# Performance work log

Measured on AMD Instinct MI355X. Metric: run time of the kernel, lower is better.

The kernel has to match this reference:

```python
import jax, jax.numpy as jnp
import numpy as np

N_NODES = 100000
IN_CH, HID_CH, OUT_CH = 128, 128, 64
N_EDGES = 1600000


def gcn_conv(x, W, b, src, dst, num_nodes):
    """PyG GCNConv: x@W -> symmetric-normalized aggregation with self-loops -> +bias."""
    h = x @ W  # [N, out]
    loop = jnp.arange(num_nodes, dtype=src.dtype)
    src_a = jnp.concatenate([src, loop])  # add self-loops
    dst_a = jnp.concatenate([dst, loop])
    # degree of destination nodes over augmented edge set (edge_weight = 1)
    deg = jax.ops.segment_sum(jnp.ones_like(dst_a, dtype=h.dtype), dst_a,
                              num_segments=num_nodes)
    dis = jnp.where(deg > 0, jax.lax.rsqrt(jnp.maximum(deg, 1e-30)), 0.0)
    norm = dis[src_a] * dis[dst_a]  # [E+N]
    msg = h[src_a] * norm[:, None]  # gather + normalize
    out = jax.ops.segment_sum(msg, dst_a, num_segments=num_nodes)  # scatter-add
    return out + b


def setup_inputs() -> dict:
    key = jax.random.key(0)
    ks = jax.random.split(key, 9)
    x = jax.random.normal(ks[0], (N_NODES, IN_CH), dtype=jnp.float32)
    edge_index = jax.random.randint(ks[1], (2, N_EDGES), 0, N_NODES, dtype=jnp.int64)
    def glorot(k, fan_in, fan_out):
        s = np.sqrt(6.0 / (fan_in + fan_out)).astype(np.float32)
        return jax.random.uniform(k, (fan_in, fan_out), jnp.float32, -s, s)
    return {
        "x": x,
        "edge_index": edge_index,
        "W1": glorot(ks[2], IN_CH, HID_CH),
        "b1": jnp.zeros((HID_CH,), jnp.float32),
        "W2": glorot(ks[3], HID_CH, HID_CH),
        "b2": jnp.zeros((HID_CH,), jnp.float32),
        "Wo": glorot(ks[4], HID_CH, OUT_CH),
        "bo": jnp.zeros((OUT_CH,), jnp.float32),
    }


def reference(x, edge_index, W1, b1, W2, b2, Wo, bo):
    src, dst = edge_index[0], edge_index[1]
    n = x.shape[0]
    x1 = jax.nn.relu(gcn_conv(x, W1, b1, src, dst, n))
    x2 = jax.nn.relu(gcn_conv(x1, W2, b2, src, dst, n))
    return (x1 + x2) @ Wo + bo
```

## Files before the change

### kernel.cpp

```cpp
#include <hip/hip_runtime.h>
#include <hip/hip_fp16.h>

#define N_NODES 100000
#define N_EDGES 1600000
#define CH 128
#define OCH 64
#define NBUCKET 391
#define CAP 8192
#define BIN_CHUNK 4096
#define ZROW N_NODES

typedef _Float16 half8 __attribute__((ext_vector_type(8)));
typedef float f32x4 __attribute__((ext_vector_type(4)));

__device__ __forceinline__ ushort f2h(float f) {
    _Float16 h = (_Float16)f;
    return *(ushort*)&h;
}

__device__ __forceinline__ uint pkadd(uint a, uint b) {
    __half2 r = __hadd2(*(__half2*)&a, *(__half2*)&b);
    return *(uint*)&r;
}

__device__ __forceinline__ uint4 pk4(uint4 a, uint4 b) {
    a.x = pkadd(a.x, b.x); a.y = pkadd(a.y, b.y);
    a.z = pkadd(a.z, b.z); a.w = pkadd(a.w, b.w);
    return a;
}

__device__ __forceinline__ int swz(int row, int k) {
    return row * 128 + ((((k >> 3) ^ (row & 15)) << 3) | (k & 7));
}


__global__ __launch_bounds__(512) void k_bin(const int* __restrict__ src,
                                             const int* __restrict__ dst,
                                             int* __restrict__ bfill,
                                             int* __restrict__ bin) {
    __shared__ int hist[512];
    __shared__ int wbase[512];
    __shared__ int cur[512];
    const int t = threadIdx.x;
    const int e0 = blockIdx.x * BIN_CHUNK;

    hist[t] = 0;
    __syncthreads();

    int ss[8], bb[8], dl[8];
#pragma unroll
    for (int j = 0; j < 8; ++j) {
        int e = e0 + j * 512 + t;
        bb[j] = -1;
        if (e < N_EDGES) {
            int s = src[e], d = dst[e];
            ss[j] = s; dl[j] = d & 255; bb[j] = d >> 8;
            atomicAdd(&hist[bb[j]], 1);
        }
    }
    __syncthreads();

    int v = hist[t];
    for (int off = 1; off < 512; off <<= 1) {
        int tv = (t >= off) ? hist[t - off] : 0;
        __syncthreads();
        hist[t] += tv;
        __syncthreads();
    }
    int excl = hist[t] - v;
    if (t < NBUCKET && v > 0) {
        int gb = atomicAdd(&bfill[t], v);
        wbase[t] = gb - excl;
    }
    cur[t] = excl;
    __syncthreads();

#pragma unroll
    for (int j = 0; j < 8; ++j) {
        if (bb[j] >= 0) {
            int p = atomicAdd(&cur[bb[j]], 1);
            bin[bb[j] * CAP + wbase[bb[j]] + p] = (ss[j] << 8) | dl[j];
        }
    }
}

__global__ __launch_bounds__(512) void k_scan_prep(const int* __restrict__ bfill,
                                                   int* __restrict__ bbase,
                                                   const float* __restrict__ W1,
                                                   const float* __restrict__ W2,
                                                   const float* __restrict__ Wo,
                                                   ushort* __restrict__ W1s,
                                                   ushort* __restrict__ W2s,
                                                   ushort* __restrict__ WoTs,
                                                   ushort* __restrict__ h) {
    if (blockIdx.x == 0) {
        __shared__ int tmp[512];
        int t = threadIdx.x;
        int v = (t < NBUCKET) ? bfill[t] : 0;
        tmp[t] = v;
        __syncthreads();
        for (int off = 1; off < 512; off <<= 1) {
            int tv = (t >= off) ? tmp[t - off] : 0;
            __syncthreads();
            tmp[t] += tv;
            __syncthreads();
        }
        if (t < NBUCKET) bbase[t] = tmp[t] - v;
    } else if (blockIdx.x == 81) {
        if (threadIdx.x < CH) h[(size_t)ZROW * CH + threadIdx.x] = 0;
    } else {
        int i = (blockIdx.x - 1) * 512 + threadIdx.x;
        if (i < 16384) {
            int k = i >> 7, n = i & 127;
            W1s[swz(n, k)] = f2h(W1[i]);
        } else if (i < 32768) {
            int j = i - 16384, k = j >> 7, n = j & 127;
            W2s[swz(n, k)] = f2h(W2[j]);
        } else if (i < 40960) {
            int j = i - 32768, k = j >> 6, n = j & 63;
            WoTs[swz(n, k)] = f2h(Wo[j]);
        }
    }
}

__global__ __launch_bounds__(256) void k_build(const int* __restrict__ bfill,
                                               const int* __restrict__ bbase,
                                               const int* __restrict__ bin,
                                               int* __restrict__ esrc,
                                               int2* __restrict__ scnt,
                                               float* __restrict__ dis) {
    __shared__ int cnt_l[256];
    __shared__ int cur_l[256];
    __shared__ int sortbuf[CAP];
    const int t = threadIdx.x;
    const int b = blockIdx.x;
    const int n = bfill[b];
    const int base = bbase[b];
    const int* brec = bin + b * CAP;

    cnt_l[t] = 0;
    __syncthreads();
    for (int i = t; i < n; i += 256)
        atomicAdd(&cnt_l[brec[i] & 255], 1);
    __syncthreads();

    int v = cnt_l[t];
    for (int off = 1; off < 256; off <<= 1) {
        int tv = (t >= off) ? cnt_l[t - off] : 0;
        __syncthreads();
        cnt_l[t] += tv;
        __syncthreads();
    }
    int excl = cnt_l[t] - v;
    int node = b * 256 + t;
    if (node < N_NODES) {
        scnt[node] = make_int2(base + excl, v);
        dis[node] = rsqrtf((float)(v + 1));
    }
    cur_l[t] = excl;
    __syncthreads();

    for (int i = t; i < n; i += 256) {
        int rec = brec[i];
        int p = atomicAdd(&cur_l[rec & 255], 1);
        sortbuf[p] = rec >> 8;
    }
    __syncthreads();
    for (int i = t; i < n; i += 256)
        esrc[base + i] = sortbuf[i];
}


template <typename IT>
__global__ __launch_bounds__(256) void k_gemm_mfma(const IT* __restrict__ A,
                                                   const ushort* __restrict__ Ws,
                                                   const float* __restrict__ dis,
                                                   ushort* __restrict__ out) {
    __shared__ ushort sB[128 * 128];
    __shared__ ushort sA[64 * 136];
    const int tid = threadIdx.x;
    const int row0 = blockIdx.x * 64;

    for (int i = tid; i < 2048; i += 256)
        ((float4*)sB)[i] = ((const float4*)Ws)[i];

    for (int i = tid; i < 2048; i += 256) {
        int m = i >> 5, u = i & 31, k4 = u << 2;
        int r = row0 + m;
        ushort4 pk = make_ushort4(0, 0, 0, 0);
        if (r < N_NODES) {
            if constexpr (sizeof(IT) == 4) {
                float4 a = ((const float4*)A)[r * 32 + u];
                pk = make_ushort4(f2h(a.x), f2h(a.y), f2h(a.z), f2h(a.w));
            } else {
                pk = ((const ushort4*)A)[r * 32 + u];
            }
        }
        *(ushort4*)&sA[swz(m, k4)] = pk;
    }
    __syncthreads();

    const int lane = tid & 63, wv = tid >> 6;
    const int mrow = lane & 15, quad = lane >> 4;
    f32x4 acc[8] = {};
#pragma unroll
    for (int kc = 0; kc < 4; ++kc) {
        int g = kc * 4 + quad;
        half8 a = *(const half8*)&sA[(wv * 16 + mrow) * 128 + ((g ^ mrow) << 3)];
#pragma unroll
        for (int nt = 0; nt < 8; ++nt) {
            half8 b = *(const half8*)&sB[(nt * 16 + mrow) * 128 + ((g ^ mrow) << 3)];
            acc[nt] = __builtin_amdgcn_mfma_f32_16x16x32_f16(a, b, acc[nt], 0, 0, 0);
        }
    }

    const int rbase4 = wv * 16 + quad * 4;
    float ds[4];
#pragma unroll
    for (int rg = 0; rg < 4; ++rg)
        ds[rg] = (row0 + rbase4 + rg < N_NODES) ? dis[row0 + rbase4 + rg] : 0.f;

    __syncthreads();
#pragma unroll
    for (int nt = 0; nt < 8; ++nt) {
#pragma unroll
        for (int rg = 0; rg < 4; ++rg)
            sA[(rbase4 + rg) * 136 + nt * 16 + mrow] = f2h(acc[nt][rg] * ds[rg]);
    }
    __syncthreads();

#pragma unroll
    for (int k = 0; k < 4; ++k) {
        int idx = tid + k * 256;
        int m = idx >> 4, c16 = idx & 15;
        int r = row0 + m;
        if (r < N_NODES) {
            uint4 vv = *(const uint4*)&sA[m * 136 + c16 * 8];
            ((uint4*)out)[(size_t)r * 16 + c16] = vv;
        }
    }
}


struct Ictx { int n; int grp; int s0, s1, s2, s3, s4, s5; };
struct Gt { uint4 t0, t1, t2, t3, t4, t5, slf; };

__device__ __forceinline__ Ictx idx_stage(const int* __restrict__ esrc, int off, int n, int q) {
    Ictx c; c.n = n;
    const int* ep = esrc + off;
    int r0 = ep[q], r1 = ep[q + 4], r2 = ep[q + 8];
    int r3 = ep[q + 12], r4 = ep[q + 16], r5 = ep[q + 20];
    bool grp = (q + 12 < n);
    bool ok = (n <= q + 24);
    c.grp = grp;
    c.s0 = (grp || q < n)      ? r0 : ZROW;
    c.s1 = (grp || q + 4 < n)  ? r1 : ZROW;
    c.s2 = (grp || q + 8 < n)  ? r2 : ZROW;
    c.s3 = grp                 ? r3 : ZROW;
    c.s4 = (grp && ok && q + 16 < n) ? r4 : ZROW;
    c.s5 = (grp && ok && q + 20 < n) ? r5 : ZROW;
    return c;
}

__device__ __forceinline__ Gt gather_stage(const Ictx& c, int v, int l,
                                           const uint4* __restrict__ h16) {
    Gt g;
    g.t0 = h16[(size_t)c.s0 * 16 + l];
    g.t1 = h16[(size_t)c.s1 * 16 + l];
    g.t2 = h16[(size_t)c.s2 * 16 + l];
    g.t3 = h16[(size_t)c.s3 * 16 + l];
    g.t4 = h16[(size_t)c.s4 * 16 + l];
    g.t5 = h16[(size_t)c.s5 * 16 + l];
    g.slf = h16[(size_t)v * 16 + l];
    return g;
}

__device__ __forceinline__ void acc_finish(const Gt& g, const Ictx& c, int v, int q, int l,
                                           const int* __restrict__ esrc, int off,
                                           const uint4* __restrict__ h16,
                                           float dsv, float4 b0, float4 b1,
                                           ushort* __restrict__ out) {
    uint4 aA = make_uint4(0, 0, 0, 0), aB = make_uint4(0, 0, 0, 0);
    aA = pk4(aA, g.t0);
    if (c.grp) aB = pk4(aB, g.t1); else aA = pk4(aA, g.t1);
    aA = pk4(aA, g.t2);
    if (c.grp) aB = pk4(aB, g.t3); else aA = pk4(aA, g.t3);
    aA = pk4(aA, g.t4);
    aA = pk4(aA, g.t5);
    if (c.n > q + 24) {
        const int* ep = esrc + off;
        int i = q + 16;
        for (; i + 12 < c.n; i += 16) {
            uint4 u0 = h16[(size_t)ep[i] * 16 + l];
            uint4 u1 = h16[(size_t)ep[i + 4] * 16 + l];
            uint4 u2 = h16[(size_t)ep[i + 8] * 16 + l];
            uint4 u3 = h16[(size_t)ep[i + 12] * 16 + l];
            aA = pk4(aA, u0); aB = pk4(aB, u1); aA = pk4(aA, u2); aB = pk4(aB, u3);
        }
        for (; i < c.n; i += 4) aA = pk4(aA, h16[(size_t)ep[i] * 16 + l]);
    }
    aA = pk4(aA, aB);
    aA.x = pkadd(aA.x, (uint)__shfl_xor((int)aA.x, 16));
    aA.y = pkadd(aA.y, (uint)__shfl_xor((int)aA.y, 16));
    aA.z = pkadd(aA.z, (uint)__shfl_xor((int)aA.z, 16));
    aA.w = pkadd(aA.w, (uint)__shfl_xor((int)aA.w, 16));
    aA.x = pkadd(aA.x, (uint)__shfl_xor((int)aA.x, 32));
    aA.y = pkadd(aA.y, (uint)__shfl_xor((int)aA.y, 32));
    aA.z = pkadd(aA.z, (uint)__shfl_xor((int)aA.z, 32));
    aA.w = pkadd(aA.w, (uint)__shfl_xor((int)aA.w, 32));

    if (q == 0) {
        aA = pk4(aA, g.slf);
        float2 a0 = __half22float2(*(__half2*)&aA.x);
        float2 a1 = __half22float2(*(__half2*)&aA.y);
        float2 a2 = __half22float2(*(__half2*)&aA.z);
        float2 a3 = __half22float2(*(__half2*)&aA.w);
        a0.x = fmaxf(a0.x * dsv + b0.x, 0.f); a0.y = fmaxf(a0.y * dsv + b0.y, 0.f);
        a1.x = fmaxf(a1.x * dsv + b0.z, 0.f); a1.y = fmaxf(a1.y * dsv + b0.w, 0.f);
        a2.x = fmaxf(a2.x * dsv + b1.x, 0.f); a2.y = fmaxf(a2.y * dsv + b1.y, 0.f);
        a3.x = fmaxf(a3.x * dsv + b1.z, 0.f); a3.y = fmaxf(a3.y * dsv + b1.w, 0.f);
        __half2 o0 = __float22half2_rn(a0);
        __half2 o1 = __float22half2_rn(a1);
        __half2 o2 = __float22half2_rn(a2);
        __half2 o3 = __float22half2_rn(a3);
        ((uint4*)out)[v * 16 + l] =
            make_uint4(*(uint*)&o0, *(uint*)&o1, *(uint*)&o2, *(uint*)&o3);
    }
}

__global__ __launch_bounds__(256) void k_agg(const int2* __restrict__ scnt,
                                             const int* __restrict__ esrc,
                                             const ushort* __restrict__ h,
                                             const float* __restrict__ dis,
                                             const float* __restrict__ bias,
                                             ushort* __restrict__ out) {
    const int w = threadIdx.x >> 6;
    const int vb = blockIdx.x * 16 + w * 4;
    const int lane = threadIdx.x & 63, q = lane >> 4, l = lane & 15;
    const uint4* h16 = (const uint4*)h;

    int2 m0 = scnt[vb], m1 = scnt[vb + 1], m2 = scnt[vb + 2], m3 = scnt[vb + 3];
    float d0 = dis[vb], d1 = dis[vb + 1], d2 = dis[vb + 2], d3 = dis[vb + 3];
    float4 b0 = ((const float4*)bias)[2 * l];
    float4 b1 = ((const float4*)bias)[2 * l + 1];

    Ictx c0 = idx_stage(esrc, m0.x, m0.y, q);
    Gt g0 = gather_stage(c0, vb, l, h16);
    Ictx c1 = idx_stage(esrc, m1.x, m1.y, q);
    Gt g1 = gather_stage(c1, vb + 1, l, h16);
    Ictx c2 = idx_stage(esrc, m2.x, m2.y, q);
    acc_finish(g0, c0, vb, q, l, esrc, m0.x, h16, d0, b0, b1, out);
    Gt g2 = gather_stage(c2, vb + 2, l, h16);
    Ictx c3 = idx_stage(esrc, m3.x, m3.y, q);
    acc_finish(g1, c1, vb + 1, q, l, esrc, m1.x, h16, d1, b0, b1, out);
    Gt g3 = gather_stage(c3, vb + 3, l, h16);
    acc_finish(g2, c2, vb + 2, q, l, esrc, m2.x, h16, d2, b0, b1, out);
    acc_finish(g3, c3, vb + 3, q, l, esrc, m3.x, h16, d3, b0, b1, out);
}


__global__ __launch_bounds__(256) void k_final_mfma(const ushort* __restrict__ x1,
                                                    const ushort* __restrict__ x2,
                                                    const ushort* __restrict__ Ws,
                                                    const float* __restrict__ bo,
                                                    float* __restrict__ out) {
    __shared__ ushort sB[64 * 128];
    __shared__ ushort sA[64 * 128];
    const int tid = threadIdx.x;
    const int row0 = blockIdx.x * 64;

    for (int i = tid; i < 1024; i += 256)
        ((float4*)sB)[i] = ((const float4*)Ws)[i];

    for (int i = tid; i < 2048; i += 256) {
        int m = i >> 5, u = i & 31, k4 = u << 2;
        int r = row0 + m;
        uint2 pk = make_uint2(0, 0);
        if (r < N_NODES) {
            uint2 ua = ((const uint2*)x1)[r * 32 + u];
            uint2 ub = ((const uint2*)x2)[r * 32 + u];
            __half2 s0 = __hadd2(*(__half2*)&ua.x, *(__half2*)&ub.x);
            __half2 s1 = __hadd2(*(__half2*)&ua.y, *(__half2*)&ub.y);
            pk = make_uint2(*(uint*)&s0, *(uint*)&s1);
        }
        *(uint2*)&sA[swz(m, k4)] = pk;
    }
    __syncthreads();

    const int lane = tid & 63, wv = tid >> 6;
    const int mrow = lane & 15, quad = lane >> 4;
    f32x4 acc[4] = {};
#pragma unroll
    for (int kc = 0; kc < 4; ++kc) {
        int g = kc * 4 + quad;
        half8 a = *(const half8*)&sA[(wv * 16 + mrow) * 128 + ((g ^ mrow) << 3)];
#pragma unroll
        for (int nt = 0; nt < 4; ++nt) {
            half8 b = *(const half8*)&sB[(nt * 16 + mrow) * 128 + ((g ^ mrow) << 3)];
            acc[nt] = __builtin_amdgcn_mfma_f32_16x16x32_f16(a, b, acc[nt], 0, 0, 0);
        }
    }

    const int rbase = row0 + wv * 16 + quad * 4;
#pragma unroll
    for (int nt = 0; nt < 4; ++nt) {
        float bb = bo[nt * 16 + mrow];
#pragma unroll
        for (int rg = 0; rg < 4; ++rg) {
            int r = rbase + rg;
            if (r < N_NODES) out[(size_t)r * 64 + nt * 16 + mrow] = acc[nt][rg] + bb;
        }
    }
}


extern "C" void kernel_launch(void* const* d_in, const int* in_sizes, int n_in,
                              void* d_out, int out_size, void* d_ws, size_t ws_size,
                              hipStream_t stream) {
    const float* x  = (const float*)d_in[0];
    const int*   ei = (const int*)d_in[1];
    const int*   src = ei;
    const int*   dst = ei + N_EDGES;
    const float* W1 = (const float*)d_in[2];
    const float* b1 = (const float*)d_in[3];
    const float* W2 = (const float*)d_in[4];
    const float* b2 = (const float*)d_in[5];
    const float* Wo = (const float*)d_in[6];
    const float* bo = (const float*)d_in[7];
    float* out = (float*)d_out;

    char* ws = (char*)d_ws;
    int*    bfill  = (int*)ws;            ws += 2048;
    int*    bbase  = (int*)ws;            ws += 2048;
    int2*   scnt   = (int2*)ws;           ws += 800000;
    float*  dis    = (float*)ws;          ws += 400000;
    int*    bin    = (int*)ws;            ws += (size_t)NBUCKET * CAP * 4;
    int*    esrc   = (int*)ws;            ws += (size_t)N_EDGES * 4;
    ushort* W1s    = (ushort*)ws;         ws += 32768;
    ushort* W2s    = (ushort*)ws;         ws += 32768;
    ushort* WoTs   = (ushort*)ws;         ws += 16384;
    ushort* h      = (ushort*)ws;         ws += (size_t)(N_NODES + 1) * CH * 2;
    ushort* x1     = (ushort*)ws;         ws += (size_t)N_NODES * CH * 2;
    ushort* x2     = (ushort*)ws;

    const int B = 256;
    const int gG = (N_NODES + 63) / 64;
    const int gA = N_NODES / 16;

    hipMemsetAsync(bfill, 0, 2048, stream);
    k_bin<<<(N_EDGES + BIN_CHUNK - 1) / BIN_CHUNK, 512, 0, stream>>>(src, dst, bfill, bin);
    k_scan_prep<<<82, 512, 0, stream>>>(bfill, bbase, W1, W2, Wo, W1s, W2s, WoTs, h);
    k_build<<<NBUCKET, 256, 0, stream>>>(bfill, bbase, bin, esrc, scnt, dis);

    k_gemm_mfma<float><<<gG, B, 0, stream>>>(x, W1s, dis, h);
    k_agg<<<gA, B, 0, stream>>>(scnt, esrc, h, dis, b1, x1);

    k_gemm_mfma<ushort><<<gG, B, 0, stream>>>(x1, W2s, dis, h);
    k_agg<<<gA, B, 0, stream>>>(scnt, esrc, h, dis, b2, x2);

    k_final_mfma<<<gG, B, 0, stream>>>(x1, x2, WoTs, bo, out);
}
```

Measured before the change: 311.4 us.

## Double GEMM row tile to 128 with 512 threads; stage final output through LDS

The dense GEMM kernels now process 128 rows per block with 512 threads, which halves the number of blocks and the per-block reloads of the weight matrix into shared memory. The final projection kernel also stages its fp32 results through shared memory, so global stores become full 16-byte row writes instead of scattered 4-byte writes. The cost is more shared memory per block (about 67KB for the GEMM), which may lower occupancy, plus an extra LDS round trip and barrier in the final kernel.

```diff
diff --git a/kernel.cpp b/kernel.cpp
--- a/kernel.cpp
+++ b/kernel.cpp
@@ -172,19 +172,19 @@
 
 
 template <typename IT>
-__global__ __launch_bounds__(256) void k_gemm_mfma(const IT* __restrict__ A,
+__global__ __launch_bounds__(512) void k_gemm_mfma(const IT* __restrict__ A,
                                                    const ushort* __restrict__ Ws,
                                                    const float* __restrict__ dis,
                                                    ushort* __restrict__ out) {
     __shared__ ushort sB[128 * 128];
-    __shared__ ushort sA[64 * 136];
+    __shared__ ushort sA[128 * 136];
     const int tid = threadIdx.x;
-    const int row0 = blockIdx.x * 64;
-
-    for (int i = tid; i < 2048; i += 256)
+    const int row0 = blockIdx.x * 128;
+
+    for (int i = tid; i < 2048; i += 512)
         ((float4*)sB)[i] = ((const float4*)Ws)[i];
 
-    for (int i = tid; i < 2048; i += 256) {
+    for (int i = tid; i < 4096; i += 512) {
         int m = i >> 5, u = i & 31, k4 = u << 2;
         int r = row0 + m;
         ushort4 pk = make_ushort4(0, 0, 0, 0);
@@ -231,7 +231,7 @@
 
 #pragma unroll
     for (int k = 0; k < 4; ++k) {
-        int idx = tid + k * 256;
+        int idx = tid + k * 512;
         int m = idx >> 4, c16 = idx & 15;
         int r = row0 + m;
         if (r < N_NODES) {
@@ -359,20 +359,21 @@
 }
 
 
-__global__ __launch_bounds__(256) void k_final_mfma(const ushort* __restrict__ x1,
+__global__ __launch_bounds__(512) void k_final_mfma(const ushort* __restrict__ x1,
                                                     const ushort* __restrict__ x2,
                                                     const ushort* __restrict__ Ws,
                                                     const float* __restrict__ bo,
                                                     float* __restrict__ out) {
     __shared__ ushort sB[64 * 128];
-    __shared__ ushort sA[64 * 128];
+    __shared__ float sF[128 * 68];
+    ushort* sA = (ushort*)sF;
     const int tid = threadIdx.x;
-    const int row0 = blockIdx.x * 64;
-
-    for (int i = tid; i < 1024; i += 256)
+    const int row0 = blockIdx.x * 128;
+
+    for (int i = tid; i < 1024; i += 512)
         ((float4*)sB)[i] = ((const float4*)Ws)[i];
 
-    for (int i = tid; i < 2048; i += 256) {
+    for (int i = tid; i < 4096; i += 512) {
         int m = i >> 5, u = i & 31, k4 = u << 2;
         int r = row0 + m;
         uint2 pk = make_uint2(0, 0);
@@ -401,14 +402,25 @@
         }
     }
 
-    const int rbase = row0 + wv * 16 + quad * 4;
+    const int rbase4 = wv * 16 + quad * 4;
+    __syncthreads();
 #pragma unroll
     for (int nt = 0; nt < 4; ++nt) {
         float bb = bo[nt * 16 + mrow];
 #pragma unroll
-        for (int rg = 0; rg < 4; ++rg) {
-            int r = rbase + rg;
-            if (r < N_NODES) out[(size_t)r * 64 + nt * 16 + mrow] = acc[nt][rg] + bb;
+        for (int rg = 0; rg < 4; ++rg)
+            sF[(rbase4 + rg) * 68 + nt * 16 + mrow] = acc[nt][rg] + bb;
+    }
+    __syncthreads();
+
+#pragma unroll
+    for (int k = 0; k < 4; ++k) {
+        int idx = tid + k * 512;
+        int m = idx >> 4, c16 = idx & 15;
+        int r = row0 + m;
+        if (r < N_NODES) {
+            uint4 vv = *(const uint4*)&sF[m * 68 + c16 * 4];
+            ((uint4*)out)[(size_t)r * 16 + c16] = vv;
         }
     }
 }
@@ -443,8 +455,7 @@
     ushort* x1     = (ushort*)ws;         ws += (size_t)N_NODES * CH * 2;
     ushort* x2     = (ushort*)ws;
 
-    const int B = 256;
-    const int gG = (N_NODES + 63) / 64;
+    const int gG = (N_NODES + 127) / 128;
     const int gA = N_NODES / 16;
 
     hipMemsetAsync(bfill, 0, 2048, stream);
@@ -452,11 +463,11 @@
     k_scan_prep<<<82, 512, 0, stream>>>(bfill, bbase, W1, W2, Wo, W1s, W2s, WoTs, h);
     k_build<<<NBUCKET, 256, 0, stream>>>(bfill, bbase, bin, esrc, scnt, dis);
 
-    k_gemm_mfma<float><<<gG, B, 0, stream>>>(x, W1s, dis, h);
-    k_agg<<<gA, B, 0, stream>>>(scnt, esrc, h, dis, b1, x1);
-
-    k_gemm_mfma<ushort><<<gG, B, 0, stream>>>(x1, W2s, dis, h);
-    k_agg<<<gA, B, 0, stream>>>(scnt, esrc, h, dis, b2, x2);
-
-    k_final_mfma<<<gG, B, 0, stream>>>(x1, x2, WoTs, bo, out);
-}
+    k_gemm_mfma<float><<<gG, 512, 0, stream>>>(x, W1s, dis, h);
+    k_agg<<<gA, 256, 0, stream>>>(scnt, esrc, h, dis, b1, x1);
+
+    k_gemm_mfma<ushort><<<gG, 512, 0, stream>>>(x1, W2s, dis, h);
+    k_agg<<<gA, 256, 0, stream>>>(scnt, esrc, h, dis, b2, x2);
+
+    k_final_mfma<<<gG, 512, 0, stream>>>(x1, x2, WoTs, bo, out);
+}
```

New measurement: 309.0 us. Within noise of the previous version (-0.8%).
